# Kernel tuning notes

Measured on AMD Instinct MI355X. Metric: run time of the kernel, lower is better.

## Reference

```python
import jax, jax.numpy as jnp
import numpy as np

N = 256
NH = 256  # GRU hidden units
K = 2     # local Hilbert space dim (hardcoded in module)


def gru_step(x, h, Wk, Wr, b):
    # TF keras GRU, reset_after=True, gate order (z, r, h)
    gx = x @ Wk + b[0]          # [B, 3*NH]
    gh = h @ Wr + b[1]          # [B, 3*NH]
    xz, xr, xh = jnp.split(gx, 3, axis=-1)
    hz, hr, hn = jnp.split(gh, 3, axis=-1)
    z = jax.nn.sigmoid(xz + hz)
    r = jax.nn.sigmoid(xr + hr)
    hh = jnp.tanh(xh + r * hn)
    return z * h + (1.0 - z) * hh


def setup_inputs() -> dict:
    key = jax.random.key(0)
    k1, k2, k3 = jax.random.split(key, 3)
    return {
        "gru_kernel": jax.random.normal(k1, (K, 3 * NH), jnp.float32) * 0.05,
        "gru_rec_kernel": jax.random.normal(k2, (NH, 3 * NH), jnp.float32) * 0.05,
        "gru_bias": jnp.zeros((2, 3 * NH), jnp.float32),
        "dense_kernel": jax.random.normal(k3, (NH, K), jnp.float32) * 0.05,
        "dense_bias": jnp.zeros((K,), jnp.float32),
        "nsamples": 2048,
    }


def reference(gru_kernel, gru_rec_kernel, gru_bias, dense_kernel, dense_bias, nsamples):
    keys = jax.random.split(jax.random.key(42), N)
    x0 = jnp.zeros((nsamples, K), jnp.float32)      # 0 * one_hot(0) == zeros
    h0 = jnp.zeros((nsamples, NH), jnp.float32)
    logP0 = jnp.zeros((nsamples,), jnp.float32)

    def step(carry, key):
        x, h, logP = carry
        h = gru_step(x, h, gru_kernel, gru_rec_kernel, gru_bias)
        probs = jax.nn.softmax(h @ dense_kernel + dense_bias, axis=-1)  # [B, K]
        log_probs = jnp.log(1e-10 + probs)
        s = jax.random.categorical(key, log_probs, axis=-1)             # [B]
        onehot = jax.nn.one_hot(s, K, dtype=jnp.float32)
        logP = logP + jnp.sum(log_probs * onehot, axis=1)
        return (onehot, h, logP), s

    (_, _, logP), samples = jax.lax.scan(step, (x0, h0, logP0), keys)
    samples = samples.T.astype(jnp.int32)  # [nsamples, N]
    return samples, logP
```

## Files before the change

### kernel.cpp

```cpp
#include <hip/hip_runtime.h>
#include <stdint.h>

#define NSTEPS 256
#define NHID   256
#define NG     768
#define BPB    8
#define TPB    768
#define NSAMP  2048

__device__ __forceinline__ uint32_t rotl32(uint32_t v, int r){ return (v<<r)|(v>>(32-r)); }

__device__ __forceinline__ void tf2x32(uint32_t k0, uint32_t k1,
                                       uint32_t x0, uint32_t x1,
                                       uint32_t& o0, uint32_t& o1){
  const uint32_t ks2 = k0 ^ k1 ^ 0x1BD11BDAu;
  x0 += k0; x1 += k1;
#define TF_R(r) { x0 += x1; x1 = rotl32(x1,(r)); x1 ^= x0; }
  TF_R(13) TF_R(15) TF_R(26) TF_R(6)
  x0 += k1;  x1 += ks2 + 1u;
  TF_R(17) TF_R(29) TF_R(16) TF_R(24)
  x0 += ks2; x1 += k0 + 2u;
  TF_R(13) TF_R(15) TF_R(26) TF_R(6)
  x0 += k0;  x1 += k1 + 3u;
  TF_R(17) TF_R(29) TF_R(16) TF_R(24)
  x0 += k1;  x1 += ks2 + 4u;
  TF_R(13) TF_R(15) TF_R(26) TF_R(6)
  x0 += ks2; x1 += k0 + 5u;
#undef TF_R
  o0 = x0; o1 = x1;
}

__device__ __forceinline__ float tanh_xla(float x){
  float xc = fminf(fmaxf(x, -9.0f), 9.0f);
  float x2 = xc*xc;
  float p = -2.76076847742355e-16f;
  p = fmaf(p, x2, 2.00018790482477e-13f);
  p = fmaf(p, x2, -8.60467152213735e-11f);
  p = fmaf(p, x2, 5.12229709037114e-08f);
  p = fmaf(p, x2, 1.48572235717979e-05f);
  p = fmaf(p, x2, 6.37261928875436e-04f);
  p = fmaf(p, x2, 4.89352455891786e-03f);
  p = p * xc;
  float q = 1.19825839466702e-06f;
  q = fmaf(q, x2, 1.18534705686654e-04f);
  q = fmaf(q, x2, 2.26843463243900e-03f);
  q = fmaf(q, x2, 4.89352518554385e-03f);
  float r = p / q;
  return (fabsf(x) < 0.0004f) ? x : r;
}

__device__ __forceinline__ float sigmoid_ref(float x){
  return fmaf(0.5f, tanh_xla(0.5f*x), 0.5f);
}

__device__ __forceinline__ void gfma(float4 h, float4 w0, float4 w1, float4 w2, float4 w3, float4& a){
  a.x = fmaf(h.x, w0.x, a.x); a.y = fmaf(h.x, w0.y, a.y);
  a.z = fmaf(h.x, w0.z, a.z); a.w = fmaf(h.x, w0.w, a.w);
  a.x = fmaf(h.y, w1.x, a.x); a.y = fmaf(h.y, w1.y, a.y);
  a.z = fmaf(h.y, w1.z, a.z); a.w = fmaf(h.y, w1.w, a.w);
  a.x = fmaf(h.z, w2.x, a.x); a.y = fmaf(h.z, w2.y, a.y);
  a.z = fmaf(h.z, w2.z, a.z); a.w = fmaf(h.z, w2.w, a.w);
  a.x = fmaf(h.w, w3.x, a.x); a.y = fmaf(h.w, w3.y, a.y);
  a.z = fmaf(h.w, w3.z, a.z); a.w = fmaf(h.w, w3.w, a.w);
}

__global__ __launch_bounds__(TPB, 3) void rnn_sampler(
    const float* __restrict__ Wk,
    const float* __restrict__ Wr,
    const float* __restrict__ Bias,
    const float* __restrict__ Dk,
    const float* __restrict__ Db,
    float* __restrict__ out)
{
  __shared__ float    h_lds[BPB][NHID];
  __shared__ float    part[4][BPB][NG];
  __shared__ uint32_t key0[NSTEPS];
  __shared__ uint32_t key1[NSTEPS];
  __shared__ float    wk_lds[2*NG];
  __shared__ float    bias_lds[2*NG];
  __shared__ float    dk_lds[NHID*2];
  __shared__ float    db_lds[2];
  __shared__ int      xsel[BPB];
  __shared__ float    logPs[BPB];

  const int tid  = threadIdx.x;
  const int b    = blockIdx.x;
  const int ks   = tid / 192;
  const int cq   = tid % 192;
  const int wid  = tid >> 6;
  const int lane = tid & 63;

  if (tid < NSTEPS) {
    uint32_t o0, o1;
    tf2x32(0u, 42u, 0u, (uint32_t)tid, o0, o1);
    key0[tid] = o0; key1[tid] = o1;
  }
  for (int i = tid; i < BPB*NHID; i += TPB) (&h_lds[0][0])[i] = 0.0f;
  for (int i = tid; i < 2*NG; i += TPB) { wk_lds[i] = Wk[i]; bias_lds[i] = Bias[i]; }
  for (int i = tid; i < NHID*2; i += TPB) dk_lds[i] = Dk[i];
  if (tid < 2) db_lds[tid] = Db[tid];
  if (tid < BPB) { xsel[tid] = 0; logPs[tid] = 0.0f; }
  __syncthreads();

  const int k0 = ks * 64;
  const float* wp = Wr + (size_t)k0 * NG + 4*cq;
  float4 acc[BPB];

  for (int t = 0; t <= NSTEPS; ++t) {
    if (t > 0 && wid < BPB) {
      const int tc = t - 1;
      const int s  = wid;
      float4 h4 = *(const float4*)&h_lds[s][lane * 4];
      float4 d0 = *(const float4*)&dk_lds[lane * 8];
      float4 d1 = *(const float4*)&dk_lds[lane * 8 + 4];
      float a0 = h4.x*d0.x + h4.y*d0.z + h4.z*d1.x + h4.w*d1.z;
      float a1 = h4.x*d0.y + h4.y*d0.w + h4.z*d1.y + h4.w*d1.w;
#pragma unroll
      for (int off = 32; off > 0; off >>= 1) {
        a0 += __shfl_down(a0, off);
        a1 += __shfl_down(a1, off);
      }
      float gv = 0.0f;
      if (lane < 2) {
        const int i = b * BPB + s;
        uint32_t o0, o1;
        tf2x32(key0[tc], key1[tc], 0u, (uint32_t)(2*i + lane), o0, o1);
        uint32_t bits = o0 ^ o1;
        const float TINY = 1.17549435e-38f;
        float u = __uint_as_float((bits >> 9) | 0x3f800000u) - 1.0f;
        u = fmaxf(TINY, u * (1.0f - TINY) + TINY);
        gv = -logf(-logf(u));
      }
      float g1 = __shfl(gv, 1);
      if (lane == 0) {
        float l0 = a0 + db_lds[0], l1 = a1 + db_lds[1];
        float m  = fmaxf(l0, l1);
        float e0 = expf(l0 - m), e1 = expf(l1 - m);
        float sum = e0 + e1;
        float p0 = e0 / sum, p1 = e1 / sum;
        float lp0 = logf(1e-10f + p0), lp1 = logf(1e-10f + p1);
        float v0 = gv + lp0, v1 = g1 + lp1;
        int st = (v1 > v0) ? 1 : 0;
        logPs[s] += st ? lp1 : lp0;
        xsel[s] = 1 + st;
        const int i = b * BPB + s;
        out[(size_t)i * NSTEPS + tc] = (float)st;
      }
    }
    if (t == NSTEPS) break;

#pragma unroll
    for (int s = 0; s < BPB; ++s) acc[s] = make_float4(0.f, 0.f, 0.f, 0.f);

    float4 wA0, wA1, wA2, wA3, wB0, wB1, wB2, wB3;
    float4 hA[BPB], hB[BPB];
    {
      const float* rp = wp;
      wA0 = *(const float4*)(rp);
      wA1 = *(const float4*)(rp + NG);
      wA2 = *(const float4*)(rp + 2*NG);
      wA3 = *(const float4*)(rp + 3*NG);
    }
#pragma unroll
    for (int s = 0; s < BPB; ++s) hA[s] = *(const float4*)&h_lds[s][k0];

    for (int g = 0; g < 16; g += 2) {
      {
        const float* rp = wp + (size_t)((g + 1) * 4) * NG;
        wB0 = *(const float4*)(rp);
        wB1 = *(const float4*)(rp + NG);
        wB2 = *(const float4*)(rp + 2*NG);
        wB3 = *(const float4*)(rp + 3*NG);
      }
#pragma unroll
      for (int s = 0; s < BPB; ++s) hB[s] = *(const float4*)&h_lds[s][k0 + 4*(g+1)];
#pragma unroll
      for (int s = 0; s < BPB; ++s) gfma(hA[s], wA0, wA1, wA2, wA3, acc[s]);

      const int g2 = (g + 2 < 16) ? (g + 2) : 0;
      {
        const float* rp = wp + (size_t)(g2 * 4) * NG;
        wA0 = *(const float4*)(rp);
        wA1 = *(const float4*)(rp + NG);
        wA2 = *(const float4*)(rp + 2*NG);
        wA3 = *(const float4*)(rp + 3*NG);
      }
#pragma unroll
      for (int s = 0; s < BPB; ++s) hA[s] = *(const float4*)&h_lds[s][k0 + 4*g2];
#pragma unroll
      for (int s = 0; s < BPB; ++s) gfma(hB[s], wB0, wB1, wB2, wB3, acc[s]);
    }

#pragma unroll
    for (int s = 0; s < BPB; ++s)
      *(float4*)&part[ks][s][4*cq] = acc[s];
    __syncthreads();

#pragma unroll
    for (int it = 0; it < 3; ++it) {
      int item;
      if (it == 0)      item = tid;
      else if (it == 1) item = tid + TPB;
      else {
        if (tid < 256) break;
        item = 1280 + tid;
      }
      int s = item >> 8, n = item & 255;
      float ghz = ((part[0][s][n]     + part[2][s][n])     + (part[1][s][n]     + part[3][s][n]))     + bias_lds[NG + n];
      float ghr = ((part[0][s][n+256] + part[2][s][n+256]) + (part[1][s][n+256] + part[3][s][n+256])) + bias_lds[NG + n + 256];
      float ghn = ((part[0][s][n+512] + part[2][s][n+512]) + (part[1][s][n+512] + part[3][s][n+512])) + bias_lds[NG + n + 512];
      int xs = xsel[s];
      float gxz, gxr, gxh;
      if (xs == 0) {
        gxz = bias_lds[n]; gxr = bias_lds[n+256]; gxh = bias_lds[n+512];
      } else {
        const float* wkrow = wk_lds + (xs - 1) * NG;
        gxz = wkrow[n]     + bias_lds[n];
        gxr = wkrow[n+256] + bias_lds[n+256];
        gxh = wkrow[n+512] + bias_lds[n+512];
      }
      float z  = sigmoid_ref(gxz + ghz);
      float r  = sigmoid_ref(gxr + ghr);
      float hh = tanh_xla(gxh + r * ghn);
      float ho = h_lds[s][n];
      h_lds[s][n] = z * ho + (1.0f - z) * hh;
    }
    __syncthreads();
  }

  __syncthreads();

  if (tid < BPB) {
    const int i = b * BPB + tid;
    out[(size_t)NSAMP * NSTEPS + i] = logPs[tid];
  }
}

extern "C" void kernel_launch(void* const* d_in, const int* in_sizes, int n_in,
                              void* d_out, int out_size, void* d_ws, size_t ws_size,
                              hipStream_t stream) {
  const float* Wk = (const float*)d_in[0];
  const float* Wr = (const float*)d_in[1];
  const float* B  = (const float*)d_in[2];
  const float* Dk = (const float*)d_in[3];
  const float* Db = (const float*)d_in[4];
  float* out = (float*)d_out;
  rnn_sampler<<<dim3(NSAMP / BPB), dim3(TPB), 0, stream>>>(Wk, Wr, B, Dk, Db, out);
}
```

Before: 3.140 ms.

## Prefetch recurrent weights across timesteps and vectorize gate update

```diff
diff --git a/kernel.cpp b/kernel.cpp
--- a/kernel.cpp
+++ b/kernel.cpp
@@ -64,6 +64,12 @@
   a.z = fmaf(h.w, w3.z, a.z); a.w = fmaf(h.w, w3.w, a.w);
 }
 
+#define LOADW(W0, W1, W2, W3, rp) { \
+  W0 = *(const float4*)(rp); \
+  W1 = *(const float4*)((rp) + NG); \
+  W2 = *(const float4*)((rp) + 2*NG); \
+  W3 = *(const float4*)((rp) + 3*NG); }
+
 __global__ __launch_bounds__(TPB, 3) void rnn_sampler(
     const float* __restrict__ Wk,
     const float* __restrict__ Wr,
@@ -104,7 +110,13 @@
 
   const int k0 = ks * 64;
   const float* wp = Wr + (size_t)k0 * NG + 4*cq;
+
+  float4 WA0, WA1, WA2, WA3, WB0, WB1, WB2, WB3;
+  LOADW(WA0, WA1, WA2, WA3, wp);
+  LOADW(WB0, WB1, WB2, WB3, wp + 4*NG);
+
   float4 acc[BPB];
+  float4 hA[BPB], hB[BPB];
 
   for (int t = 0; t <= NSTEPS; ++t) {
     if (t > 0 && wid < BPB) {
@@ -151,44 +163,36 @@
 
 #pragma unroll
     for (int s = 0; s < BPB; ++s) acc[s] = make_float4(0.f, 0.f, 0.f, 0.f);
-
-    float4 wA0, wA1, wA2, wA3, wB0, wB1, wB2, wB3;
-    float4 hA[BPB], hB[BPB];
+#pragma unroll
+    for (int s = 0; s < BPB; ++s) hA[s] = *(const float4*)&h_lds[s][k0];
+
+    const float* rpA = wp + (size_t)8 * NG;
+    const float* rpB = wp + (size_t)12 * NG;
+#pragma unroll 1
+    for (int p = 0; p < 7; ++p) {
+      const int g = 2 * p;
+#pragma unroll
+      for (int s = 0; s < BPB; ++s) hB[s] = *(const float4*)&h_lds[s][k0 + 4*(g+1)];
+#pragma unroll
+      for (int s = 0; s < BPB; ++s) gfma(hA[s], WA0, WA1, WA2, WA3, acc[s]);
+      LOADW(WA0, WA1, WA2, WA3, rpA);
+      rpA += 8 * NG;
+#pragma unroll
+      for (int s = 0; s < BPB; ++s) hA[s] = *(const float4*)&h_lds[s][k0 + 4*(g+2)];
+#pragma unroll
+      for (int s = 0; s < BPB; ++s) gfma(hB[s], WB0, WB1, WB2, WB3, acc[s]);
+      LOADW(WB0, WB1, WB2, WB3, rpB);
+      rpB += 8 * NG;
+    }
     {
-      const float* rp = wp;
-      wA0 = *(const float4*)(rp);
-      wA1 = *(const float4*)(rp + NG);
-      wA2 = *(const float4*)(rp + 2*NG);
-      wA3 = *(const float4*)(rp + 3*NG);
-    }
-#pragma unroll
-    for (int s = 0; s < BPB; ++s) hA[s] = *(const float4*)&h_lds[s][k0];
-
-    for (int g = 0; g < 16; g += 2) {
-      {
-        const float* rp = wp + (size_t)((g + 1) * 4) * NG;
-        wB0 = *(const float4*)(rp);
-        wB1 = *(const float4*)(rp + NG);
-        wB2 = *(const float4*)(rp + 2*NG);
-        wB3 = *(const float4*)(rp + 3*NG);
-      }
-#pragma unroll
-      for (int s = 0; s < BPB; ++s) hB[s] = *(const float4*)&h_lds[s][k0 + 4*(g+1)];
-#pragma unroll
-      for (int s = 0; s < BPB; ++s) gfma(hA[s], wA0, wA1, wA2, wA3, acc[s]);
-
-      const int g2 = (g + 2 < 16) ? (g + 2) : 0;
-      {
-        const float* rp = wp + (size_t)(g2 * 4) * NG;
-        wA0 = *(const float4*)(rp);
-        wA1 = *(const float4*)(rp + NG);
-        wA2 = *(const float4*)(rp + 2*NG);
-        wA3 = *(const float4*)(rp + 3*NG);
-      }
-#pragma unroll
-      for (int s = 0; s < BPB; ++s) hA[s] = *(const float4*)&h_lds[s][k0 + 4*g2];
-#pragma unroll
-      for (int s = 0; s < BPB; ++s) gfma(hB[s], wB0, wB1, wB2, wB3, acc[s]);
+#pragma unroll
+      for (int s = 0; s < BPB; ++s) hB[s] = *(const float4*)&h_lds[s][k0 + 4*15];
+#pragma unroll
+      for (int s = 0; s < BPB; ++s) gfma(hA[s], WA0, WA1, WA2, WA3, acc[s]);
+      LOADW(WA0, WA1, WA2, WA3, wp);
+#pragma unroll
+      for (int s = 0; s < BPB; ++s) gfma(hB[s], WB0, WB1, WB2, WB3, acc[s]);
+      LOADW(WB0, WB1, WB2, WB3, wp + 4*NG);
     }
 
 #pragma unroll
@@ -196,34 +200,50 @@
       *(float4*)&part[ks][s][4*cq] = acc[s];
     __syncthreads();
 
-#pragma unroll
-    for (int it = 0; it < 3; ++it) {
-      int item;
-      if (it == 0)      item = tid;
-      else if (it == 1) item = tid + TPB;
-      else {
-        if (tid < 256) break;
-        item = 1280 + tid;
-      }
-      int s = item >> 8, n = item & 255;
-      float ghz = ((part[0][s][n]     + part[2][s][n])     + (part[1][s][n]     + part[3][s][n]))     + bias_lds[NG + n];
-      float ghr = ((part[0][s][n+256] + part[2][s][n+256]) + (part[1][s][n+256] + part[3][s][n+256])) + bias_lds[NG + n + 256];
-      float ghn = ((part[0][s][n+512] + part[2][s][n+512]) + (part[1][s][n+512] + part[3][s][n+512])) + bias_lds[NG + n + 512];
-      int xs = xsel[s];
-      float gxz, gxr, gxh;
-      if (xs == 0) {
-        gxz = bias_lds[n]; gxr = bias_lds[n+256]; gxh = bias_lds[n+512];
-      } else {
+    if (tid < 512) {
+      const int s = tid >> 6;
+      const int n = (tid & 63) << 2;
+      float4 pz0 = *(const float4*)&part[0][s][n];
+      float4 pz2 = *(const float4*)&part[2][s][n];
+      float4 pz1 = *(const float4*)&part[1][s][n];
+      float4 pz3 = *(const float4*)&part[3][s][n];
+      float4 pr0 = *(const float4*)&part[0][s][n+256];
+      float4 pr2 = *(const float4*)&part[2][s][n+256];
+      float4 pr1 = *(const float4*)&part[1][s][n+256];
+      float4 pr3 = *(const float4*)&part[3][s][n+256];
+      float4 pn0 = *(const float4*)&part[0][s][n+512];
+      float4 pn2 = *(const float4*)&part[2][s][n+512];
+      float4 pn1 = *(const float4*)&part[1][s][n+512];
+      float4 pn3 = *(const float4*)&part[3][s][n+512];
+      float4 bhz = *(const float4*)&bias_lds[NG + n];
+      float4 bhr = *(const float4*)&bias_lds[NG + n + 256];
+      float4 bhn = *(const float4*)&bias_lds[NG + n + 512];
+      float4 gxz = *(const float4*)&bias_lds[n];
+      float4 gxr = *(const float4*)&bias_lds[n + 256];
+      float4 gxh = *(const float4*)&bias_lds[n + 512];
+      const int xs = xsel[s];
+      if (xs != 0) {
         const float* wkrow = wk_lds + (xs - 1) * NG;
-        gxz = wkrow[n]     + bias_lds[n];
-        gxr = wkrow[n+256] + bias_lds[n+256];
-        gxh = wkrow[n+512] + bias_lds[n+512];
-      }
-      float z  = sigmoid_ref(gxz + ghz);
-      float r  = sigmoid_ref(gxr + ghr);
-      float hh = tanh_xla(gxh + r * ghn);
-      float ho = h_lds[s][n];
-      h_lds[s][n] = z * ho + (1.0f - z) * hh;
+        float4 w0 = *(const float4*)&wkrow[n];
+        float4 w1 = *(const float4*)&wkrow[n + 256];
+        float4 w2 = *(const float4*)&wkrow[n + 512];
+        gxz.x = w0.x + gxz.x; gxz.y = w0.y + gxz.y; gxz.z = w0.z + gxz.z; gxz.w = w0.w + gxz.w;
+        gxr.x = w1.x + gxr.x; gxr.y = w1.y + gxr.y; gxr.z = w1.z + gxr.z; gxr.w = w1.w + gxr.w;
+        gxh.x = w2.x + gxh.x; gxh.y = w2.y + gxh.y; gxh.z = w2.z + gxh.z; gxh.w = w2.w + gxh.w;
+      }
+      float4 ho = *(const float4*)&h_lds[s][n];
+      float4 hnew;
+#define GCOMP(c) { \
+      float ghz = ((pz0.c + pz2.c) + (pz1.c + pz3.c)) + bhz.c; \
+      float ghr = ((pr0.c + pr2.c) + (pr1.c + pr3.c)) + bhr.c; \
+      float ghn = ((pn0.c + pn2.c) + (pn1.c + pn3.c)) + bhn.c; \
+      float zg = sigmoid_ref(gxz.c + ghz); \
+      float rg = sigmoid_ref(gxr.c + ghr); \
+      float hh = tanh_xla(gxh.c + rg * ghn); \
+      hnew.c = zg * ho.c + (1.0f - zg) * hh; }
+      GCOMP(x) GCOMP(y) GCOMP(z) GCOMP(w)
+#undef GCOMP
+      *(float4*)&h_lds[s][n] = hnew;
     }
     __syncthreads();
   }
```

New measurement: 5.234 ms. 1.67x slower.
